# Optimization experiments

Hardware: AMD Instinct MI355X
Metric: run time of the kernel (lower is better)

Reference implementation:

```python
import jax, jax.numpy as jnp
import numpy as np

B, S = 256, 500
NQ, DQ, DV, M, F = 10000, 128, 256, 50, 512


def _kaiming(key, shape, fan_in):
    return jax.random.normal(key, shape, dtype=jnp.float32) * np.sqrt(2.0 / fan_in)


def setup_inputs() -> dict:
    key = jax.random.key(0)
    ks = jax.random.split(key, 24)
    inp = {
        'q_data': jax.random.randint(ks[0], (B, S), 0, NQ, dtype=jnp.int32),
        'qa_data': jax.random.randint(ks[1], (B, S), 0, 2 * NQ, dtype=jnp.int32),
        'target': jax.random.randint(ks[2], (B, S), 0, 3, dtype=jnp.int32),
        'time_data': jax.random.randint(ks[3], (B, S), 0, 9902, dtype=jnp.int32),
        'attempt_data': jax.random.randint(ks[4], (B, S), 0, 4000, dtype=jnp.int32),
        'hint_data': jax.random.randint(ks[5], (B, S), 0, 60, dtype=jnp.int32),
        'hintTotal_data': jax.random.randint(ks[6], (B, S), 0, 60, dtype=jnp.int32),
    }
    # embedding tables (padding row 0 zeroed, as in torch padding_idx=0)
    inp['q_emb'] = _kaiming(ks[7], (NQ + 1, DQ), DQ).at[0].set(0.0)
    inp['qa_emb'] = _kaiming(ks[8], (2 * NQ + 1, DV), DV).at[0].set(0.0)
    inp['time_emb'] = _kaiming(ks[9], (9902, DQ), DQ).at[0].set(0.0)
    inp['attempt_emb'] = _kaiming(ks[10], (4000, DQ), DQ).at[0].set(0.0)
    inp['hint_total_emb'] = _kaiming(ks[11], (60, DQ), DQ).at[0].set(0.0)
    # memory init
    inp['Mk'] = _kaiming(ks[12], (M, DQ), DQ)
    inp['Mv0'] = _kaiming(ks[13], (M, DV), DV)
    # difficulty linears (shared weights applied twice)
    inp['diff_W'] = _kaiming(ks[14], (DQ, DQ), DQ)
    inp['diff_b'] = jnp.zeros((DQ,), jnp.float32)
    inp['diff2_W'] = _kaiming(ks[15], (DQ, DQ), DQ)
    inp['diff2_b'] = jnp.zeros((DQ,), jnp.float32)
    # DKVMN write head: erase/add linears (DV -> DV)
    inp['erase_W'] = _kaiming(ks[16], (DV, DV), DV)
    inp['erase_b'] = jnp.zeros((DV,), jnp.float32)
    inp['add_W'] = _kaiming(ks[17], (DV, DV), DV)
    inp['add_b'] = jnp.zeros((DV,), jnp.float32)
    # readout
    inp['read_W'] = _kaiming(ks[18], (F, DV + DQ), DV + DQ)
    inp['read_b'] = jnp.zeros((F,), jnp.float32)
    inp['pred_W'] = _kaiming(ks[19], (1, F), F)
    inp['pred_b'] = jnp.zeros((1,), jnp.float32)
    return inp


def reference(q_data, qa_data, target, time_data, attempt_data, hint_data, hintTotal_data,
              q_emb, qa_emb, time_emb, attempt_emb, hint_total_emb,
              Mk, Mv0, diff_W, diff_b, diff2_W, diff2_b,
              erase_W, erase_b, add_W, add_b, read_W, read_b, pred_W, pred_b):
    lin1 = lambda x: x @ diff_W.T + diff_b
    lin2 = lambda x: x @ diff2_W.T + diff2_b

    qe = q_emb[q_data]                        # [B,S,DQ]
    te = time_emb[time_data]
    ae = attempt_emb[attempt_data]
    he = hint_total_emb[hint_data]            # forward uses hint_total_embed for both
    hte = hint_total_emb[hintTotal_data]

    time_final = jax.nn.sigmoid(lin2(jnp.tanh(lin1(te + qe))))
    diff_final = jax.nn.sigmoid(lin2(jnp.tanh(lin1(hte + he + ae + qe))))
    q_proc = lin1(qe + diff_final * (he + hte + ae))  # [B,S,DQ]
    qa_e = qa_emb[qa_data]                            # [B,S,DV]

    Mv_init = jnp.broadcast_to(Mv0[None], (q_data.shape[0], M, DV))

    def step(Mv, inp):
        q, qa = inp                                   # [B,DQ], [B,DV]
        w = jax.nn.softmax(q @ Mk.T, axis=-1)         # [B,M]
        read = jnp.einsum('bm,bmd->bd', w, Mv)        # [B,DV]
        e = jax.nn.sigmoid(qa @ erase_W.T + erase_b)  # [B,DV]
        a = jnp.tanh(qa @ add_W.T + add_b)            # [B,DV]
        Mv = Mv * (1.0 - w[:, :, None] * e[:, None, :]) + w[:, :, None] * a[:, None, :]
        return Mv, read

    _, reads = jax.lax.scan(step, Mv_init,
                            (jnp.swapaxes(q_proc, 0, 1), jnp.swapaxes(qa_e, 0, 1)))
    reads = jnp.swapaxes(reads, 0, 1)                 # [B,S,DV]

    input_embed = q_proc + time_final * te            # [B,S,DQ]
    predict_input = jnp.concatenate([reads, input_embed], axis=-1)
    rc = jnp.tanh(predict_input @ read_W.T + read_b)  # [B,S,F]
    pred = (rc @ pred_W.T + pred_b).reshape(-1)       # [B*S]

    t1 = target.reshape(-1)
    mask = t1 >= 1
    y = jnp.where(mask, t1 - 1, 0).astype(jnp.float32)
    # BCE with logits: log(1+e^x) - x*y
    lelem = jnp.logaddexp(0.0, pred) - pred * y
    n = jnp.maximum(jnp.sum(mask.astype(jnp.float32)), 1.0)
    loss = jnp.sum(jnp.where(mask, lelem, 0.0)) / n
    maskf = mask.astype(jnp.float32)
    return loss, jax.nn.sigmoid(pred) * maskf, y * maskf
```

## Files before the change

### kernel.cpp

```cpp
#include <hip/hip_runtime.h>
#include <cstdint>
#include <cstddef>

#define NB 256
#define SQ 500
#define NROWS (NB * SQ)
#define DQ 128
#define DV 256
#define MM 50
#define FF 512
#define NQA 20096
#define WSTRIDE 52
#define WT 10

typedef _Float16 half8 __attribute__((ext_vector_type(8)));
typedef float floatx4 __attribute__((ext_vector_type(4)));
typedef float f2 __attribute__((ext_vector_type(2)));
typedef unsigned int u32;
typedef unsigned short u16;

typedef __attribute__((address_space(1))) void gvoid;
typedef __attribute__((address_space(3))) void lvoid;

__device__ __forceinline__ void gl16(const u16* g, u16* l) {
    __builtin_amdgcn_global_load_lds((gvoid*)g, (lvoid*)l, 16, 0, 0);
}

__device__ __forceinline__ float4 ld4(const float* p) {
    return *reinterpret_cast<const float4*>(p);
}
__device__ __forceinline__ float sigf(float x) { return 1.f / (1.f + __expf(-x)); }
__device__ __forceinline__ float tanhfast(float x) { return 2.f / (1.f + __expf(-2.f * x)) - 1.f; }
__device__ __forceinline__ int gmap(int l, int s0, int CS) {
    int b = (unsigned)l / (unsigned)CS;
    return b * SQ + s0 + (l - b * CS);
}
__device__ __forceinline__ void st4h(u16* dst, float4 v) {
    _Float16 h0 = (_Float16)v.x, h1 = (_Float16)v.y, h2 = (_Float16)v.z, h3 = (_Float16)v.w;
    ushort4 u;
    u.x = *(u16*)&h0; u.y = *(u16*)&h1; u.z = *(u16*)&h2; u.w = *(u16*)&h3;
    *(ushort4*)dst = u;
}
__device__ __forceinline__ float h2f(u16 b) { _Float16 h; *(u16*)&h = b; return (float)h; }
__device__ __forceinline__ u16 f2h(float x) { _Float16 h = (_Float16)x; return *(u16*)&h; }

__global__ __launch_bounds__(256) void cvt16(
    const float* __restrict__ s, u16* __restrict__ d, int n4)
{
    int i = blockIdx.x * 256 + threadIdx.x;
    if (i < n4) st4h(d + 4 * (size_t)i, ld4(s + 4 * (size_t)i));
}

__global__ __launch_bounds__(256) void wcvt(
    const float* __restrict__ s0, const float* __restrict__ s1,
    const float* __restrict__ s2, const float* __restrict__ s3,
    const float* __restrict__ s4, u16* __restrict__ dst)
{
    int i = blockIdx.x * 256 + threadIdx.x;
    if (i >= 90112) return;
    const float* s; int off;
    if (i < 4096)       { s = s0; off = 0; }
    else if (i < 8192)  { s = s1; off = 4096; }
    else if (i < 24576) { s = s2; off = 8192; }
    else if (i < 40960) { s = s3; off = 24576; }
    else                { s = s4; off = 40960; }
    st4h(dst + 4 * (size_t)i, ld4(s + 4 * (size_t)(i - off)));
}

__global__ __launch_bounds__(256) void mkcvt(
    const float* __restrict__ Mk, u16* __restrict__ Mkh)
{
    int i = blockIdx.x * 256 + threadIdx.x;
    if (i >= 64 * 32) return;
    int row = i >> 5;
    float4 v = (row < MM) ? ld4(Mk + (size_t)row * DQ + (i & 31) * 4)
                          : float4{0.f, 0.f, 0.f, 0.f};
    st4h(Mkh + 4 * (size_t)i, v);
}

__global__ __launch_bounds__(256) void prep128(
    const int* __restrict__ q_data, const int* __restrict__ time_data,
    const int* __restrict__ attempt_data, const int* __restrict__ hint_data,
    const int* __restrict__ hintT_data,
    const float* __restrict__ q_emb, const float* __restrict__ time_emb,
    const float* __restrict__ attempt_emb, const float* __restrict__ ht_emb,
    u16* __restrict__ Xp, u16* __restrict__ RDIE,
    int s0, int CS, int Nc)
{
    int g = blockIdx.x * 256 + threadIdx.x;
    int l = g >> 5;
    int kq = (g & 31) << 2;
    if (l >= Nc) return;
    int n = gmap(l, s0, CS);
    float4 qe  = ld4(q_emb       + (size_t)q_data[n]       * DQ + kq);
    float4 te  = ld4(time_emb    + (size_t)time_data[n]    * DQ + kq);
    float4 ae  = ld4(attempt_emb + (size_t)attempt_data[n] * DQ + kq);
    float4 he  = ld4(ht_emb      + (size_t)hint_data[n]    * DQ + kq);
    float4 hte = ld4(ht_emb      + (size_t)hintT_data[n]   * DQ + kq);
    size_t off = (size_t)l * DQ + kq;
    float4 x1, s3, x2;
    x1.x = te.x + qe.x; x1.y = te.y + qe.y; x1.z = te.z + qe.z; x1.w = te.w + qe.w;
    s3.x = he.x + hte.x + ae.x; s3.y = he.y + hte.y + ae.y;
    s3.z = he.z + hte.z + ae.z; s3.w = he.w + hte.w + ae.w;
    x2.x = s3.x + qe.x; x2.y = s3.y + qe.y; x2.z = s3.z + qe.z; x2.w = s3.w + qe.w;
    st4h(Xp + off, x1);
    st4h(Xp + (size_t)Nc * DQ + off, x2);
    st4h(RDIE + (size_t)l * 384 + kq, qe);
    st4h(RDIE + (size_t)l * 384 + 128 + kq, s3);
}

__global__ __launch_bounds__(256, 2) void gemm12(
    const u16* __restrict__ A, const u16* __restrict__ W1h,
    const u16* __restrict__ W2h, const float* __restrict__ b1,
    const float* __restrict__ b2, u16* __restrict__ Yh,
    const u16* __restrict__ RDIE, int Nc)
{
    __shared__ u16 smem[32768];
    u16* At = smem;
    u16* Bt = smem + 8192;
    u16* Tt = smem + 16384;
    const int tid = threadIdx.x;
    const int row0 = blockIdx.x * 128;
    const int lane = tid & 63, wv = tid >> 6;
    const int wr = (wv >> 1) * 64, wc = (wv & 1) * 64;
    const int q = lane >> 4, c0 = lane & 15;

    floatx4 acc[4][4];
#pragma unroll
    for (int m = 0; m < 4; ++m)
#pragma unroll
        for (int n = 0; n < 4; ++n) acc[m][n] = (floatx4)0.f;

    for (int kt = 0; kt < 128; kt += 64) {
#pragma unroll
        for (int j = 0; j < 4; ++j) {
            int f = tid + j * 256; int r = f >> 3; int lg = (f & 7) ^ (r & 7);
            gl16(A + (size_t)(row0 + r) * 128 + kt + lg * 8, &At[f * 8]);
        }
#pragma unroll
        for (int j = 0; j < 4; ++j) {
            int f = tid + j * 256; int r = f >> 3; int lg = (f & 7) ^ (r & 7);
            gl16(W1h + (size_t)r * 128 + kt + lg * 8, &Bt[f * 8]);
        }
        __syncthreads();
#pragma unroll
        for (int kk = 0; kk < 2; ++kk) {
            half8 af[4], bf[4];
#pragma unroll
            for (int m = 0; m < 4; ++m) {
                int row = wr + m * 16 + c0;
                af[m] = *(half8*)&At[row * 64 + ((((kk << 2) | q)) ^ (row & 7)) * 8];
            }
#pragma unroll
            for (int n = 0; n < 4; ++n) {
                int row = wc + n * 16 + c0;
                bf[n] = *(half8*)&Bt[row * 64 + ((((kk << 2) | q)) ^ (row & 7)) * 8];
            }
#pragma unroll
            for (int m = 0; m < 4; ++m)
#pragma unroll
                for (int n = 0; n < 4; ++n)
                    acc[m][n] = __builtin_amdgcn_mfma_f32_16x16x32_f16(af[m], bf[n], acc[m][n], 0, 0, 0);
        }
        __syncthreads();
    }

    {
        float bv1[4];
#pragma unroll
        for (int n = 0; n < 4; ++n) bv1[n] = b1[wc + n * 16 + c0];
#pragma unroll
        for (int m = 0; m < 4; ++m)
#pragma unroll
            for (int r4 = 0; r4 < 4; ++r4) {
                int row = wr + m * 16 + q * 4 + r4;
#pragma unroll
                for (int n = 0; n < 4; ++n) {
                    int col = wc + n * 16 + c0;
                    float v = tanhfast(acc[m][n][r4] + bv1[n]);
                    int tile = col >> 6, cl = col & 63, gl = cl >> 3;
                    Tt[tile * 8192 + row * 64 + ((gl ^ (row & 7)) << 3) + (cl & 7)] = f2h(v);
                }
            }
    }
#pragma unroll
    for (int m = 0; m < 4; ++m)
#pragma unroll
        for (int n = 0; n < 4; ++n) acc[m][n] = (floatx4)0.f;

#pragma unroll
    for (int j = 0; j < 4; ++j) {
        int f = tid + j * 256; int r = f >> 3; int lg = (f & 7) ^ (r & 7);
        gl16(W2h + (size_t)r * 128 + 0 + lg * 8, &Bt[f * 8]);
    }
    __syncthreads();

#pragma unroll
    for (int kt = 0; kt < 2; ++kt) {
#pragma unroll
        for (int kk = 0; kk < 2; ++kk) {
            half8 af[4], bf[4];
#pragma unroll
            for (int m = 0; m < 4; ++m) {
                int row = wr + m * 16 + c0;
                af[m] = *(half8*)&Tt[kt * 8192 + row * 64 + ((((kk << 2) | q)) ^ (row & 7)) * 8];
            }
#pragma unroll
            for (int n = 0; n < 4; ++n) {
                int row = wc + n * 16 + c0;
                bf[n] = *(half8*)&Bt[row * 64 + ((((kk << 2) | q)) ^ (row & 7)) * 8];
            }
#pragma unroll
            for (int m = 0; m < 4; ++m)
#pragma unroll
                for (int n = 0; n < 4; ++n)
                    acc[m][n] = __builtin_amdgcn_mfma_f32_16x16x32_f16(af[m], bf[n], acc[m][n], 0, 0, 0);
        }
        if (kt == 0) {
            __syncthreads();
#pragma unroll
            for (int j = 0; j < 4; ++j) {
                int f = tid + j * 256; int r = f >> 3; int lg = (f & 7) ^ (r & 7);
                gl16(W2h + (size_t)r * 128 + 64 + lg * 8, &Bt[f * 8]);
            }
            __syncthreads();
        }
    }

    float bv[4];
#pragma unroll
    for (int n = 0; n < 4; ++n) bv[n] = b2[wc + n * 16 + c0];
#pragma unroll
    for (int m = 0; m < 4; ++m)
#pragma unroll
        for (int r4 = 0; r4 < 4; ++r4) {
            int row = row0 + wr + m * 16 + q * 4 + r4;
#pragma unroll
            for (int n = 0; n < 4; ++n) {
                int col = wc + n * 16 + c0;
                float v = sigf(acc[m][n][r4] + bv[n]);
                if (row < Nc) {
                    Yh[(size_t)row * 128 + col] = f2h(v);
                } else {
                    size_t o = (size_t)(row - Nc) * 384 + col;
                    float qe = h2f(RDIE[o]), s3 = h2f(RDIE[o + 128]);
                    Yh[(size_t)row * 128 + col] = f2h(fmaf(v, s3, qe));
                }
            }
        }
}

__global__ __launch_bounds__(256, 2) void gemm3w(
    const u16* __restrict__ X3, const u16* __restrict__ W1h,
    const float* __restrict__ b1, const u16* __restrict__ Mkh,
    const int* __restrict__ tidx, const float* __restrict__ temb,
    const u16* __restrict__ TF, u16* __restrict__ RDIE,
    float* __restrict__ Wb, int s0, int CS)
{
    __shared__ u16 smem[32768];
    u16* At = smem;
    u16* Bt = smem + 8192;
    u16* Tt = smem + 16384;
    const int tid = threadIdx.x;
    const int row0 = blockIdx.x * 128;
    const int lane = tid & 63, wv = tid >> 6;
    const int wr = (wv >> 1) * 64, wc = (wv & 1) * 64;
    const int q = lane >> 4, c0 = lane & 15;

    floatx4 acc[4][4];
#pragma unroll
    for (int m = 0; m < 4; ++m)
#pragma unroll
        for (int n = 0; n < 4; ++n) acc[m][n] = (floatx4)0.f;

    for (int kt = 0; kt < 128; kt += 64) {
#pragma unroll
        for (int j = 0; j < 4; ++j) {
            int f = tid + j * 256; int r = f >> 3; int lg = (f & 7) ^ (r & 7);
            gl16(X3 + (size_t)(row0 + r) * 128 + kt + lg * 8, &At[f * 8]);
        }
#pragma unroll
        for (int j = 0; j < 4; ++j) {
            int f = tid + j * 256; int r = f >> 3; int lg = (f & 7) ^ (r & 7);
            gl16(W1h + (size_t)r * 128 + kt + lg * 8, &Bt[f * 8]);
        }
        __syncthreads();
#pragma unroll
        for (int kk = 0; kk < 2; ++kk) {
            half8 af[4], bf[4];
#pragma unroll
            for (int m = 0; m < 4; ++m) {
                int row = wr + m * 16 + c0;
                af[m] = *(half8*)&At[row * 64 + ((((kk << 2) | q)) ^ (row & 7)) * 8];
            }
#pragma unroll
            for (int n = 0; n < 4; ++n) {
                int row = wc + n * 16 + c0;
                bf[n] = *(half8*)&Bt[row * 64 + ((((kk << 2) | q)) ^ (row & 7)) * 8];
            }
#pragma unroll
            for (int m = 0; m < 4; ++m)
#pragma unroll
                for (int n = 0; n < 4; ++n)
                    acc[m][n] = __builtin_amdgcn_mfma_f32_16x16x32_f16(af[m], bf[n], acc[m][n], 0, 0, 0);
        }
        __syncthreads();
    }

    {
        float bv1[4];
#pragma unroll
        for (int n = 0; n < 4; ++n) bv1[n] = b1[wc + n * 16 + c0];
#pragma unroll
        for (int m = 0; m < 4; ++m)
#pragma unroll
            for (int r4 = 0; r4 < 4; ++r4) {
                int rloc = wr + m * 16 + q * 4 + r4;
                int grow = row0 + rloc;
                int nmap = gmap(grow, s0, CS);
                const float* terow = temb + (size_t)tidx[nmap] * 128;
#pragma unroll
                for (int n = 0; n < 4; ++n) {
                    int col = wc + n * 16 + c0;
                    float qp = acc[m][n][r4] + bv1[n];
                    int tile = col >> 6, cl = col & 63, gl = cl >> 3;
                    Tt[tile * 8192 + rloc * 64 + ((gl ^ (rloc & 7)) << 3) + (cl & 7)] = f2h(qp);
                    float tf = h2f(TF[(size_t)grow * 128 + col]);
                    RDIE[(size_t)grow * 384 + 256 + col] = f2h(fmaf(tf, terow[col], qp));
                }
            }
    }
#pragma unroll
    for (int j = 0; j < 4; ++j) {
        int f = tid + j * 256;
        int fl = f & 511;
        int ktile = f >> 9;
        int r = fl >> 3;
        int lg = (fl & 7) ^ (r & 7);
        gl16(Mkh + (size_t)r * 128 + ktile * 64 + lg * 8, &Bt[f * 8]);
    }
    __syncthreads();

    const int wrW = wv * 32;
    floatx4 acc2[2][4];
#pragma unroll
    for (int m = 0; m < 2; ++m)
#pragma unroll
        for (int n = 0; n < 4; ++n) acc2[m][n] = (floatx4)0.f;
#pragma unroll
    for (int kt = 0; kt < 2; ++kt)
#pragma unroll
        for (int kk = 0; kk < 2; ++kk) {
            half8 af[2], bf[4];
#pragma unroll
            for (int m = 0; m < 2; ++m) {
                int row = wrW + m * 16 + c0;
                af[m] = *(half8*)&Tt[kt * 8192 + row * 64 + ((((kk << 2) | q)) ^ (row & 7)) * 8];
            }
#pragma unroll
            for (int n = 0; n < 4; ++n) {
                int row = n * 16 + c0;
                bf[n] = *(half8*)&Bt[kt * 4096 + row * 64 + ((((kk << 2) | q)) ^ (row & 7)) * 8];
            }
#pragma unroll
            for (int m = 0; m < 2; ++m)
#pragma unroll
                for (int n = 0; n < 4; ++n)
                    acc2[m][n] = __builtin_amdgcn_mfma_f32_16x16x32_f16(af[m], bf[n], acc2[m][n], 0, 0, 0);
        }
    __syncthreads();

    float* Sred = (float*)smem;
#pragma unroll
    for (int m = 0; m < 2; ++m)
#pragma unroll
        for (int r4 = 0; r4 < 4; ++r4) {
            int row = wrW + m * 16 + q * 4 + r4;
#pragma unroll
            for (int n = 0; n < 4; ++n)
                Sred[row * 67 + n * 16 + c0] = acc2[m][n][r4];
        }
    __syncthreads();

    if (tid < 128) {
        float* s = &Sred[tid * 67];
        float mx = -3.0e38f;
#pragma unroll
        for (int m = 0; m < MM; ++m) mx = fmaxf(mx, s[m]);
        float sum = 0.f;
#pragma unroll
        for (int m = 0; m < MM; ++m) { float e = __expf(s[m] - mx); s[m] = e; sum += e; }
        float inv = 1.f / sum;
#pragma unroll
        for (int m = 0; m < MM; ++m) s[m] *= inv;
        s[50] = 0.f; s[51] = 0.f;
    }
    __syncthreads();

    for (int i = tid; i < 128 * 13; i += 256) {
        int row = i / 13, seg = i - row * 13;
        float4 v;
        v.x = Sred[row * 67 + seg * 4 + 0];
        v.y = Sred[row * 67 + seg * 4 + 1];
        v.z = Sred[row * 67 + seg * 4 + 2];
        v.w = Sred[row * 67 + seg * 4 + 3];
        *(float4*)(Wb + (size_t)(row0 + row) * WSTRIDE + seg * 4) = v;
    }
}

template <int MODE>
__global__ __launch_bounds__(256, 4) void gemm16(
    const u16* __restrict__ A, const u16* __restrict__ W0,
    const u16* __restrict__ W1, const float* __restrict__ b0,
    const float* __restrict__ b1, u16* __restrict__ Yh,
    float* __restrict__ Yf,
    u16* __restrict__ AUX, const float* __restrict__ predW,
    int K)
{
    __shared__ u16 smem[2 * 128 * 64];
    u16* At = smem;
    u16* Bt = smem + 128 * 64;
    const int tid = threadIdx.x;
    const int row0 = blockIdx.y * 128;
    const int by = blockIdx.x;

    const u16* Wp;
    int col0;
    if constexpr (MODE == 4) { Wp = (by < 2) ? W0 : W1; col0 = (by & 1) * 128; }
    else { Wp = W0; col0 = by * 128; }
    const float* bias = (MODE == 4 && by >= 2) ? b1 : b0;

    floatx4 acc[4][4];
#pragma unroll
    for (int m = 0; m < 4; ++m)
#pragma unroll
        for (int n = 0; n < 4; ++n) acc[m][n] = (floatx4)0.f;

    const int lane = tid & 63, wv = tid >> 6;
    const int wr = (wv >> 1) * 64, wc = (wv & 1) * 64;
    const int q = lane >> 4, c0 = lane & 15;

    for (int kt = 0; kt < K; kt += 64) {
#pragma unroll
        for (int j = 0; j < 4; ++j) {
            int f = tid + j * 256;
            int r = f >> 3;
            int lg = (f & 7) ^ (r & 7);
            gl16(A + (size_t)(row0 + r) * K + kt + lg * 8, &At[f * 8]);
        }
#pragma unroll
        for (int j = 0; j < 4; ++j) {
            int f = tid + j * 256;
            int r = f >> 3;
            int lg = (f & 7) ^ (r & 7);
            gl16(Wp + (size_t)(col0 + r) * K + kt + lg * 8, &Bt[f * 8]);
        }
        __syncthreads();
#pragma unroll
        for (int kk = 0; kk < 2; ++kk) {
            half8 af[4], bf[4];
#pragma unroll
            for (int m = 0; m < 4; ++m) {
                int row = wr + m * 16 + c0;
                af[m] = *(half8*)&At[row * 64 + ((((kk << 2) | q)) ^ (row & 7)) * 8];
            }
#pragma unroll
            for (int n = 0; n < 4; ++n) {
                int row = wc + n * 16 + c0;
                bf[n] = *(half8*)&Bt[row * 64 + ((((kk << 2) | q)) ^ (row & 7)) * 8];
            }
#pragma unroll
            for (int m = 0; m < 4; ++m)
#pragma unroll
                for (int n = 0; n < 4; ++n)
                    acc[m][n] = __builtin_amdgcn_mfma_f32_16x16x32_f16(af[m], bf[n], acc[m][n], 0, 0, 0);
        }
        __syncthreads();
    }

    float bv[4];
#pragma unroll
    for (int n = 0; n < 4; ++n) bv[n] = bias[col0 + wc + n * 16 + c0];

    if constexpr (MODE == 5) {
        float pw[4];
#pragma unroll
        for (int n = 0; n < 4; ++n) pw[n] = predW[col0 + wc + n * 16 + c0];
        float* red = (float*)smem;
#pragma unroll
        for (int m = 0; m < 4; ++m)
#pragma unroll
            for (int r4 = 0; r4 < 4; ++r4) {
                int row = wr + m * 16 + q * 4 + r4;
                float pp = 0.f;
#pragma unroll
                for (int n = 0; n < 4; ++n)
                    pp = fmaf(tanhfast(acc[m][n][r4] + bv[n]), pw[n], pp);
                red[row * 33 + (wv & 1) * 16 + c0] = pp;
            }
        __syncthreads();
        if (tid < 128) {
            float s = 0.f;
#pragma unroll
            for (int j = 0; j < 32; ++j) s += red[tid * 33 + j];
            Yf[(size_t)(row0 + tid) * 4 + by] = s;
        }
    } else {
#pragma unroll
        for (int m = 0; m < 4; ++m)
#pragma unroll
            for (int r4 = 0; r4 < 4; ++r4) {
                int row = row0 + wr + m * 16 + q * 4 + r4;
#pragma unroll
                for (int n = 0; n < 4; ++n) {
                    int col = col0 + wc + n * 16 + c0;
                    float v = acc[m][n][r4] + bv[n];
                    bool isE = (by < 2);
                    v = isE ? sigf(v) : tanhfast(v);
                    AUX[((size_t)row * 256 + col) * 2 + (isE ? 0 : 1)] = f2h(v);
                }
            }
    }
}

__global__ __launch_bounds__(256, 1) void scan_kernel(
    const float* __restrict__ Wb, const int* __restrict__ qa_data,
    const u32* __restrict__ EAtab,
    const float* __restrict__ Mv0, float* __restrict__ MvSt,
    u16* __restrict__ RDIE, int CS, int s0, int first)
{
    __shared__ float wt[2][WT * WSTRIDE];
    const int b = blockIdx.x;
    const int d = threadIdx.x;

    f2 mv[25];
    if (first) {
#pragma unroll
        for (int j = 0; j < 25; ++j) {
            mv[j].x = Mv0[(2 * j) * DV + d];
            mv[j].y = Mv0[(2 * j + 1) * DV + d];
        }
    } else {
#pragma unroll
        for (int j = 0; j < 25; ++j) {
            mv[j].x = MvSt[((size_t)b * MM + 2 * j) * DV + d];
            mv[j].y = MvSt[((size_t)b * MM + 2 * j + 1) * DV + d];
        }
    }

    const float* wbase = Wb + (size_t)b * CS * WSTRIDE;
    const int* qap = qa_data + (size_t)b * SQ + s0;
    u16* rp = RDIE + (size_t)b * CS * 384 + d;

    const int NT = CS / WT;
    const bool loader = (d < (WT * WSTRIDE / 4));

    if (loader) *(float4*)&wt[0][d * 4] = ld4(wbase + d * 4);
    u32 ea[WT];
    {
        int qi[WT];
#pragma unroll
        for (int i = 0; i < WT; ++i) qi[i] = qap[i];
#pragma unroll
        for (int i = 0; i < WT; ++i) ea[i] = EAtab[(size_t)qi[i] * DV + d];
    }
    __syncthreads();

    int cur = 0;
    for (int tile = 0; tile < NT; ++tile) {
        float4 wreg;
        u32 ean[WT];
        const bool havenext = (tile + 1 < NT);
        if (havenext) {
            if (loader) wreg = ld4(wbase + (size_t)(tile + 1) * WT * WSTRIDE + d * 4);
            int qn[WT];
#pragma unroll
            for (int i = 0; i < WT; ++i) qn[i] = qap[(tile + 1) * WT + i];
#pragma unroll
            for (int i = 0; i < WT; ++i) ean[i] = EAtab[(size_t)qn[i] * DV + d];
        }

        float4 wpp[2][13];
#pragma unroll
        for (int i = 0; i < 13; ++i)
            wpp[0][i] = *(const float4*)&wt[cur][i * 4];

#pragma unroll
        for (int s = 0; s < WT; ++s) {
            if (s + 1 < WT) {
#pragma unroll
                for (int i = 0; i < 13; ++i)
                    wpp[(s + 1) & 1][i] =
                        *(const float4*)&wt[cur][(s + 1) * WSTRIDE + i * 4];
            }
            const f2* w2 = (const f2*)wpp[s & 1];
            u32 eav = ea[s];
            float e = h2f((u16)(eav & 0xffff));
            float a = h2f((u16)(eav >> 16));
            f2 e2; e2.x = e; e2.y = e;
            f2 a2; a2.x = a; a2.y = a;
            f2 r0 = (f2)0.f, r1 = (f2)0.f, r2 = (f2)0.f, r3 = (f2)0.f;
#pragma unroll
            for (int j = 0; j < 24; j += 4) {
                f2 w_0 = w2[j + 0], w_1 = w2[j + 1], w_2 = w2[j + 2], w_3 = w2[j + 3];
                r0 += w_0 * mv[j + 0];
                r1 += w_1 * mv[j + 1];
                r2 += w_2 * mv[j + 2];
                r3 += w_3 * mv[j + 3];
                f2 t0 = a2 - e2 * mv[j + 0];
                f2 t1 = a2 - e2 * mv[j + 1];
                f2 t2 = a2 - e2 * mv[j + 2];
                f2 t3 = a2 - e2 * mv[j + 3];
                mv[j + 0] += w_0 * t0;
                mv[j + 1] += w_1 * t1;
                mv[j + 2] += w_2 * t2;
                mv[j + 3] += w_3 * t3;
            }
            {
                f2 w24 = w2[24];
                r0 += w24 * mv[24];
                f2 t = a2 - e2 * mv[24];
                mv[24] += w24 * t;
            }
            f2 rs = (r0 + r1) + (r2 + r3);
            rp[(size_t)(tile * WT + s) * 384] = f2h(rs.x + rs.y);
        }

        if (havenext) {
            if (loader) *(float4*)&wt[1 - cur][d * 4] = wreg;
#pragma unroll
            for (int i = 0; i < WT; ++i) ea[i] = ean[i];
            __syncthreads();
            cur ^= 1;
        }
    }

#pragma unroll
    for (int j = 0; j < 25; ++j) {
        MvSt[((size_t)b * MM + 2 * j) * DV + d]     = mv[j].x;
        MvSt[((size_t)b * MM + 2 * j + 1) * DV + d] = mv[j].y;
    }
}

__global__ __launch_bounds__(256) void loss_part(
    const float* __restrict__ P4, const int* __restrict__ target,
    const float* __restrict__ pred_b, float* __restrict__ out,
    float* __restrict__ R2, int s0, int CS, int Nc)
{
    int l = blockIdx.x * 256 + threadIdx.x;
    float le = 0.f, mf = 0.f;
    if (l < Nc) {
        int n = gmap(l, s0, CS);
        float4 p4 = ld4(P4 + (size_t)l * 4);
        float p = (p4.x + p4.y) + (p4.z + p4.w) + pred_b[0];
        int t = target[n];
        float y = (t >= 1) ? (float)(t - 1) : 0.f;
        float sig = 1.f / (1.f + __expf(-p));
        if (t >= 1) {
            mf = 1.f;
            le = fmaxf(p, 0.f) + log1pf(__expf(-fabsf(p))) - p * y;
        }
        out[1 + n] = sig * mf;
        out[1 + NROWS + n] = y * mf;
    }
#pragma unroll
    for (int off = 32; off; off >>= 1) {
        le += __shfl_down(le, off);
        mf += __shfl_down(mf, off);
    }
    __shared__ float sl[4], sm[4];
    int wid = threadIdx.x >> 6;
    if ((threadIdx.x & 63) == 0) { sl[wid] = le; sm[wid] = mf; }
    __syncthreads();
    if (threadIdx.x == 0) {
        atomicAdd(R2, sl[0] + sl[1] + sl[2] + sl[3]);
        atomicAdd(R2 + 1, sm[0] + sm[1] + sm[2] + sm[3]);
    }
}

__global__ void loss_fin(const float* __restrict__ R2, float* __restrict__ out)
{
    out[0] = R2[0] / fmaxf(R2[1], 1.f);
}

extern "C" void kernel_launch(void* const* d_in, const int* in_sizes, int n_in,
                              void* d_out, int out_size, void* d_ws, size_t ws_size,
                              hipStream_t stream)
{
    const int* q_data       = (const int*)d_in[0];
    const int* qa_data      = (const int*)d_in[1];
    const int* target       = (const int*)d_in[2];
    const int* time_data    = (const int*)d_in[3];
    const int* attempt_data = (const int*)d_in[4];
    const int* hint_data    = (const int*)d_in[5];
    const int* hintT_data   = (const int*)d_in[6];
    const float* q_emb    = (const float*)d_in[7];
    const float* qa_emb   = (const float*)d_in[8];
    const float* time_emb = (const float*)d_in[9];
    const float* att_emb  = (const float*)d_in[10];
    const float* ht_emb   = (const float*)d_in[11];
    const float* Mk       = (const float*)d_in[12];
    const float* Mv0      = (const float*)d_in[13];
    const float* diff_W   = (const float*)d_in[14];
    const float* diff_b   = (const float*)d_in[15];
    const float* diff2_W  = (const float*)d_in[16];
    const float* diff2_b  = (const float*)d_in[17];
    const float* erase_W  = (const float*)d_in[18];
    const float* erase_b  = (const float*)d_in[19];
    const float* add_W    = (const float*)d_in[20];
    const float* add_b    = (const float*)d_in[21];
    const float* read_W   = (const float*)d_in[22];
    const float* read_b   = (const float*)d_in[23];
    const float* pred_W   = (const float*)d_in[24];
    const float* pred_b   = (const float*)d_in[25];
    float* out = (float*)d_out;
    (void)in_sizes; (void)n_in; (void)out_size;

    static const int cs_opts[] = {500, 250, 100, 50, 20, 10};
    const size_t FIXED = 44800000ull;
    int CS = 0;
    for (int i = 0; i < 6; ++i) {
        size_t need = (size_t)NB * cs_opts[i] * 1504ull + FIXED;
        if (need <= ws_size) { CS = cs_opts[i]; break; }
    }
    if (CS == 0) return;
    const int NCH = SQ / CS;
    const int Nc = NB * CS;

    float* MvSt  = (float*)d_ws;
    float* wbuf  = MvSt + (size_t)NB * MM * DV;
    float* bufP4 = wbuf + (size_t)Nc * WSTRIDE;
    float* bufR2 = bufP4 + (size_t)Nc * 4;
    u16*  Xp     = (u16*)(bufR2 + 4);
    u16*  RDIE   = Xp + (size_t)2 * Nc * 128;
    u16*  dWh    = RDIE + (size_t)Nc * 384;
    u16*  d2Wh   = dWh + 16384;
    u16*  eWh    = d2Wh + 16384;
    u16*  aWh    = eWh + 65536;
    u16*  rWh    = aWh + 65536;
    u16*  qaEh   = rWh + 196608;
    u16*  Mkh    = qaEh + 5120256;
    u32*  EAtab  = (u32*)(Mkh + 8192);

    wcvt<<<352, 256, 0, stream>>>(diff_W, diff2_W, erase_W, add_W, read_W, dWh);
    cvt16<<<5001, 256, 0, stream>>>(qa_emb, qaEh, 5120256 / 4);
    mkcvt<<<8, 256, 0, stream>>>(Mk, Mkh);
    hipMemsetAsync(bufR2, 0, 4 * sizeof(float), stream);

    gemm16<4><<<dim3(4, NQA / 128), 256, 0, stream>>>(
        qaEh, eWh, aWh, erase_b, add_b, nullptr, nullptr,
        (u16*)EAtab, nullptr, 256);

    for (int c = 0; c < NCH; ++c) {
        const int s0 = c * CS;

        prep128<<<Nc / 8, 256, 0, stream>>>(
            q_data, time_data, attempt_data, hint_data, hintT_data,
            q_emb, time_emb, att_emb, ht_emb, Xp, RDIE, s0, CS, Nc);

        gemm12<<<2 * Nc / 128, 256, 0, stream>>>(
            Xp, dWh, d2Wh, diff_b, diff2_b, Xp, RDIE, Nc);

        gemm3w<<<Nc / 128, 256, 0, stream>>>(
            Xp + (size_t)Nc * 128, dWh, diff_b, Mkh,
            time_data, time_emb, Xp, RDIE, wbuf, s0, CS);

        scan_kernel<<<NB, DV, 0, stream>>>(
            wbuf, qa_data, EAtab, Mv0, MvSt, RDIE, CS, s0, c == 0 ? 1 : 0);

        gemm16<5><<<dim3(4, Nc / 128), 256, 0, stream>>>(
            RDIE, rWh, nullptr, read_b, nullptr, nullptr, bufP4,
            nullptr, pred_W, 384);

        loss_part<<<Nc / 256, 256, 0, stream>>>(bufP4, target, pred_b, out, bufR2, s0, CS, Nc);
    }

    loss_fin<<<1, 1, 0, stream>>>(bufR2, out);
}
```

Before: 610.5 us.

## Split scan memory slots across two thread halves with shared-memory read reduction

The scan kernel now launches 512 threads per batch row instead of 256. Each half owns roughly half of the 50 memory slots (12 or 13 pairs), so the serial per-step work per thread is roughly halved and each compute unit gets more waves. Partial read sums from the two halves go into a shared buffer and are combined after a barrier for every tile of steps. The cost is an extra barrier and shared-memory traffic per tile. The mv load/store loops now use a runtime bound, which risks dynamic register indexing or scratch spills.

```diff
diff --git a/kernel.cpp b/kernel.cpp
--- a/kernel.cpp
+++ b/kernel.cpp
@@ -523,39 +523,42 @@
     }
 }
 
-__global__ __launch_bounds__(256, 1) void scan_kernel(
+__global__ __launch_bounds__(512, 2) void scan_kernel(
     const float* __restrict__ Wb, const int* __restrict__ qa_data,
     const u32* __restrict__ EAtab,
     const float* __restrict__ Mv0, float* __restrict__ MvSt,
     u16* __restrict__ RDIE, int CS, int s0, int first)
 {
     __shared__ float wt[2][WT * WSTRIDE];
+    __shared__ float part[WT][2][256];
     const int b = blockIdx.x;
-    const int d = threadIdx.x;
-
-    f2 mv[25];
+    const int tid = threadIdx.x;
+    const int half = tid >> 8;
+    const int d = tid & 255;
+    const int mbase = half ? 24 : 0;
+    const int npair = half ? 13 : 12;
+
+    f2 mv[13];
     if (first) {
-#pragma unroll
-        for (int j = 0; j < 25; ++j) {
-            mv[j].x = Mv0[(2 * j) * DV + d];
-            mv[j].y = Mv0[(2 * j + 1) * DV + d];
+        for (int j = 0; j < npair; ++j) {
+            mv[j].x = Mv0[(mbase + 2 * j) * DV + d];
+            mv[j].y = Mv0[(mbase + 2 * j + 1) * DV + d];
         }
     } else {
-#pragma unroll
-        for (int j = 0; j < 25; ++j) {
-            mv[j].x = MvSt[((size_t)b * MM + 2 * j) * DV + d];
-            mv[j].y = MvSt[((size_t)b * MM + 2 * j + 1) * DV + d];
+        for (int j = 0; j < npair; ++j) {
+            mv[j].x = MvSt[((size_t)b * MM + mbase + 2 * j) * DV + d];
+            mv[j].y = MvSt[((size_t)b * MM + mbase + 2 * j + 1) * DV + d];
         }
     }
 
     const float* wbase = Wb + (size_t)b * CS * WSTRIDE;
     const int* qap = qa_data + (size_t)b * SQ + s0;
-    u16* rp = RDIE + (size_t)b * CS * 384 + d;
+    u16* rpB = RDIE + (size_t)b * CS * 384;
 
     const int NT = CS / WT;
-    const bool loader = (d < (WT * WSTRIDE / 4));
-
-    if (loader) *(float4*)&wt[0][d * 4] = ld4(wbase + d * 4);
+    const bool loader = (tid < (WT * WSTRIDE / 4));
+
+    if (loader) *(float4*)&wt[0][tid * 4] = ld4(wbase + tid * 4);
     u32 ea[WT];
     {
         int qi[WT];
@@ -572,7 +575,7 @@
         u32 ean[WT];
         const bool havenext = (tile + 1 < NT);
         if (havenext) {
-            if (loader) wreg = ld4(wbase + (size_t)(tile + 1) * WT * WSTRIDE + d * 4);
+            if (loader) wreg = ld4(wbase + (size_t)(tile + 1) * WT * WSTRIDE + tid * 4);
             int qn[WT];
 #pragma unroll
             for (int i = 0; i < WT; ++i) qn[i] = qap[(tile + 1) * WT + i];
@@ -580,54 +583,97 @@
             for (int i = 0; i < WT; ++i) ean[i] = EAtab[(size_t)qn[i] * DV + d];
         }
 
-        float4 wpp[2][13];
-#pragma unroll
-        for (int i = 0; i < 13; ++i)
-            wpp[0][i] = *(const float4*)&wt[cur][i * 4];
-
-#pragma unroll
-        for (int s = 0; s < WT; ++s) {
-            if (s + 1 < WT) {
-#pragma unroll
-                for (int i = 0; i < 13; ++i)
-                    wpp[(s + 1) & 1][i] =
-                        *(const float4*)&wt[cur][(s + 1) * WSTRIDE + i * 4];
-            }
-            const f2* w2 = (const f2*)wpp[s & 1];
-            u32 eav = ea[s];
-            float e = h2f((u16)(eav & 0xffff));
-            float a = h2f((u16)(eav >> 16));
-            f2 e2; e2.x = e; e2.y = e;
-            f2 a2; a2.x = a; a2.y = a;
-            f2 r0 = (f2)0.f, r1 = (f2)0.f, r2 = (f2)0.f, r3 = (f2)0.f;
-#pragma unroll
-            for (int j = 0; j < 24; j += 4) {
-                f2 w_0 = w2[j + 0], w_1 = w2[j + 1], w_2 = w2[j + 2], w_3 = w2[j + 3];
-                r0 += w_0 * mv[j + 0];
-                r1 += w_1 * mv[j + 1];
-                r2 += w_2 * mv[j + 2];
-                r3 += w_3 * mv[j + 3];
-                f2 t0 = a2 - e2 * mv[j + 0];
-                f2 t1 = a2 - e2 * mv[j + 1];
-                f2 t2 = a2 - e2 * mv[j + 2];
-                f2 t3 = a2 - e2 * mv[j + 3];
-                mv[j + 0] += w_0 * t0;
-                mv[j + 1] += w_1 * t1;
-                mv[j + 2] += w_2 * t2;
-                mv[j + 3] += w_3 * t3;
-            }
-            {
-                f2 w24 = w2[24];
-                r0 += w24 * mv[24];
-                f2 t = a2 - e2 * mv[24];
-                mv[24] += w24 * t;
-            }
-            f2 rs = (r0 + r1) + (r2 + r3);
-            rp[(size_t)(tile * WT + s) * 384] = f2h(rs.x + rs.y);
+        if (half == 0) {
+            float4 wpp[2][6];
+#pragma unroll
+            for (int i = 0; i < 6; ++i) wpp[0][i] = *(const float4*)&wt[cur][i * 4];
+#pragma unroll
+            for (int s = 0; s < WT; ++s) {
+                if (s + 1 < WT) {
+#pragma unroll
+                    for (int i = 0; i < 6; ++i)
+                        wpp[(s + 1) & 1][i] = *(const float4*)&wt[cur][(s + 1) * WSTRIDE + i * 4];
+                }
+                const f2* w2 = (const f2*)wpp[s & 1];
+                u32 eav = ea[s];
+                float e = h2f((u16)(eav & 0xffff));
+                float a = h2f((u16)(eav >> 16));
+                f2 e2; e2.x = e; e2.y = e;
+                f2 a2; a2.x = a; a2.y = a;
+                f2 r0 = (f2)0.f, r1 = (f2)0.f, r2 = (f2)0.f, r3 = (f2)0.f;
+#pragma unroll
+                for (int j = 0; j < 12; j += 4) {
+                    f2 w_0 = w2[j + 0], w_1 = w2[j + 1], w_2 = w2[j + 2], w_3 = w2[j + 3];
+                    r0 += w_0 * mv[j + 0];
+                    r1 += w_1 * mv[j + 1];
+                    r2 += w_2 * mv[j + 2];
+                    r3 += w_3 * mv[j + 3];
+                    f2 t0 = a2 - e2 * mv[j + 0];
+                    f2 t1 = a2 - e2 * mv[j + 1];
+                    f2 t2 = a2 - e2 * mv[j + 2];
+                    f2 t3 = a2 - e2 * mv[j + 3];
+                    mv[j + 0] += w_0 * t0;
+                    mv[j + 1] += w_1 * t1;
+                    mv[j + 2] += w_2 * t2;
+                    mv[j + 3] += w_3 * t3;
+                }
+                f2 rs = (r0 + r1) + (r2 + r3);
+                part[s][0][d] = rs.x + rs.y;
+            }
+        } else {
+            float4 wpp[2][7];
+#pragma unroll
+            for (int i = 0; i < 7; ++i) wpp[0][i] = *(const float4*)&wt[cur][24 + i * 4];
+#pragma unroll
+            for (int s = 0; s < WT; ++s) {
+                if (s + 1 < WT) {
+#pragma unroll
+                    for (int i = 0; i < 7; ++i)
+                        wpp[(s + 1) & 1][i] = *(const float4*)&wt[cur][(s + 1) * WSTRIDE + 24 + i * 4];
+                }
+                const f2* w2 = (const f2*)wpp[s & 1];
+                u32 eav = ea[s];
+                float e = h2f((u16)(eav & 0xffff));
+                float a = h2f((u16)(eav >> 16));
+                f2 e2; e2.x = e; e2.y = e;
+                f2 a2; a2.x = a; a2.y = a;
+                f2 r0 = (f2)0.f, r1 = (f2)0.f, r2 = (f2)0.f, r3 = (f2)0.f;
+#pragma unroll
+                for (int j = 0; j < 12; j += 4) {
+                    f2 w_0 = w2[j + 0], w_1 = w2[j + 1], w_2 = w2[j + 2], w_3 = w2[j + 3];
+                    r0 += w_0 * mv[j + 0];
+                    r1 += w_1 * mv[j + 1];
+                    r2 += w_2 * mv[j + 2];
+                    r3 += w_3 * mv[j + 3];
+                    f2 t0 = a2 - e2 * mv[j + 0];
+                    f2 t1 = a2 - e2 * mv[j + 1];
+                    f2 t2 = a2 - e2 * mv[j + 2];
+                    f2 t3 = a2 - e2 * mv[j + 3];
+                    mv[j + 0] += w_0 * t0;
+                    mv[j + 1] += w_1 * t1;
+                    mv[j + 2] += w_2 * t2;
+                    mv[j + 3] += w_3 * t3;
+                }
+                {
+                    f2 w12 = w2[12];
+                    r0 += w12 * mv[12];
+                    f2 t = a2 - e2 * mv[12];
+                    mv[12] += w12 * t;
+                }
+                f2 rs = (r0 + r1) + (r2 + r3);
+                part[s][1][d] = rs.x + rs.y;
+            }
+        }
+        __syncthreads();
+
+        for (int i = tid; i < WT * 256; i += 512) {
+            int s = i >> 8, dd = i & 255;
+            float r = part[s][0][dd] + part[s][1][dd];
+            rpB[(size_t)(tile * WT + s) * 384 + dd] = f2h(r);
         }
 
         if (havenext) {
-            if (loader) *(float4*)&wt[1 - cur][d * 4] = wreg;
+            if (loader) *(float4*)&wt[1 - cur][tid * 4] = wreg;
 #pragma unroll
             for (int i = 0; i < WT; ++i) ea[i] = ean[i];
             __syncthreads();
@@ -635,10 +681,9 @@
         }
     }
 
-#pragma unroll
-    for (int j = 0; j < 25; ++j) {
-        MvSt[((size_t)b * MM + 2 * j) * DV + d]     = mv[j].x;
-        MvSt[((size_t)b * MM + 2 * j + 1) * DV + d] = mv[j].y;
+    for (int j = 0; j < npair; ++j) {
+        MvSt[((size_t)b * MM + mbase + 2 * j) * DV + d]     = mv[j].x;
+        MvSt[((size_t)b * MM + mbase + 2 * j + 1) * DV + d] = mv[j].y;
     }
 }
 
@@ -765,7 +810,7 @@
             Xp + (size_t)Nc * 128, dWh, diff_b, Mkh,
             time_data, time_emb, Xp, RDIE, wbuf, s0, CS);
 
-        scan_kernel<<<NB, DV, 0, stream>>>(
+        scan_kernel<<<NB, 512, 0, stream>>>(
             wbuf, qa_data, EAtab, Mv0, MvSt, RDIE, CS, s0, c == 0 ? 1 : 0);
 
         gemm16<5><<<dim3(4, Nc / 128), 256, 0, stream>>>(
```

New measurement: 702.3 us. +15.0%, slower.
